# Kernel optimization log

Measured on AMD Instinct MI355X. Metric: run time of the kernel, lower is better.

Reference implementation:

```python
import jax, jax.numpy as jnp
import numpy as np

TEMPERATURE = 0.07


def setup_inputs() -> dict:
    key = jax.random.key(0)
    embeddings = jax.random.normal(key, (16384, 256), dtype=jnp.float32)
    return {"embeddings": embeddings}


def reference(embeddings) -> jnp.ndarray:
    # L2 normalize rows (torch F.normalize uses eps clamp 1e-12)
    norm = jnp.maximum(jnp.linalg.norm(embeddings, axis=1, keepdims=True), 1e-12)
    emb = embeddings / norm
    # [N, N] similarity, temperature-scaled logits
    logits = jnp.matmul(emb, emb.T) / TEMPERATURE
    # cross entropy against diagonal labels (labels[i] = i)
    logp = jax.nn.log_softmax(logits, axis=1)
    loss = -jnp.mean(jnp.diagonal(logp))
    return loss
```

## Files before the change

kernel.cpp:

```cpp
#include <hip/hip_runtime.h>
#include <hip/hip_bf16.h>

typedef __bf16 bf16;
typedef __attribute__((ext_vector_type(8))) __bf16 bf16x8;
typedef __attribute__((ext_vector_type(4))) __bf16 bf16x4;
typedef __attribute__((ext_vector_type(16))) float f32x16;

#define N_ROWS 16384
#define DIM 256
#define NJC 512
#define LSTRIP 16
#define NSTRIPS 2112
#define SQK1 4.53981608f
#define LN2F 0.69314718056f

#define WS_T_OFF (N_ROWS * DIM * 2)
#define WS_D_OFF (WS_T_OFF + N_ROWS * 4)

#define GLOAD_LDS(g, l)                                        \
    __builtin_amdgcn_global_load_lds(                          \
        (const __attribute__((address_space(1))) void*)(g),    \
        (__attribute__((address_space(3))) void*)(l), 16, 0, 0)

__global__ void __launch_bounds__(256) normalize_kernel(const float* __restrict__ in,
                                                        bf16* __restrict__ out,
                                                        float* __restrict__ Tg,
                                                        float* __restrict__ Dg,
                                                        float* __restrict__ loss_out) {
    if (blockIdx.x == 0 && threadIdx.x == 0) loss_out[0] = 0.0f;
    if (blockIdx.x < 64) Tg[blockIdx.x * 256 + threadIdx.x] = 0.0f;

    const int row  = blockIdx.x * 4 + (threadIdx.x >> 6);
    const int lane = threadIdx.x & 63;
    const float4* rp = (const float4*)(in + (size_t)row * DIM);
    float4 v = rp[lane];
    float ss = v.x * v.x + v.y * v.y + v.z * v.z + v.w * v.w;
#pragma unroll
    for (int m = 1; m < 64; m <<= 1) ss += __shfl_xor(ss, m, 64);
    float inv = SQK1 / fmaxf(sqrtf(ss), 1e-12f);
    bf16x4 o;
    o[0] = (bf16)(v.x * inv);
    o[1] = (bf16)(v.y * inv);
    o[2] = (bf16)(v.z * inv);
    o[3] = (bf16)(v.w * inv);
    *(bf16x4*)(out + (size_t)row * DIM + lane * 4) = o;

    float f0 = (float)o[0], f1 = (float)o[1], f2 = (float)o[2], f3 = (float)o[3];
    float s2 = f0 * f0 + f1 * f1 + f2 * f2 + f3 * f3;
#pragma unroll
    for (int m = 1; m < 64; m <<= 1) s2 += __shfl_xor(s2, m, 64);
    if (lane == 0) Dg[row] = s2;
}

#define TREE16(R, out)                                                     \
    do {                                                                   \
        float w8[8], w4[4], w2[2], w1, g_;                                 \
        _Pragma("unroll") for (int i_ = 0; i_ < 8; ++i_) {                 \
            g_ = (lo & 16) ? R[i_] : R[i_ + 8];                            \
            w8[i_] = ((lo & 16) ? R[i_ + 8] : R[i_]) + __shfl_xor(g_, 16); \
        }                                                                  \
        _Pragma("unroll") for (int i_ = 0; i_ < 4; ++i_) {                 \
            g_ = (lo & 8) ? w8[i_] : w8[i_ + 4];                           \
            w4[i_] = ((lo & 8) ? w8[i_ + 4] : w8[i_]) + __shfl_xor(g_, 8); \
        }                                                                  \
        _Pragma("unroll") for (int i_ = 0; i_ < 2; ++i_) {                 \
            g_ = (lo & 4) ? w4[i_] : w4[i_ + 2];                           \
            w2[i_] = ((lo & 4) ? w4[i_ + 2] : w4[i_]) + __shfl_xor(g_, 4); \
        }                                                                  \
        g_ = (lo & 2) ? w2[0] : w2[1];                                     \
        w1 = ((lo & 2) ? w2[1] : w2[0]) + __shfl_xor(g_, 2);               \
        out = w1 + __shfl_xor(w1, 1);                                      \
    } while (0)

__global__ void __launch_bounds__(256, 4)
loss_kernel(const bf16* __restrict__ A, float* __restrict__ Tg) {
    __shared__ bf16 Bs0[32 * DIM];
    __shared__ bf16 Bs1[32 * DIM];

    const int tid = threadIdx.x;
    const int w  = tid >> 6;
    const int l  = tid & 63;
    const int lo = l & 31, hi = l >> 5;

    int it = 0, rem = blockIdx.x;
    for (;;) {
        const int nch = 32 - (it >> 2);
        if (rem < nch) break;
        rem -= nch;
        ++it;
    }
    const int jc0 = 4 * it + rem * LSTRIP;
    const int jc1 = (jc0 + LSTRIP < NJC) ? (jc0 + LSTRIP) : NJC;

    bf16x8 af[16];
    {
        const bf16* ap = A + (size_t)(it * 128 + w * 32 + lo) * DIM + hi * 8;
#pragma unroll
        for (int k = 0; k < 16; ++k)
            af[k] = *(const volatile bf16x8*)(ap + k * 16);
    }

    float s0[16];
#pragma unroll
    for (int r = 0; r < 16; ++r) s0[r] = 0.f;

    const int s_dma = l & 31;
    const int rl    = l >> 5;
    int vo[4];
#pragma unroll
    for (int q = 0; q < 4; ++q) {
        const int c = (s_dma & 24) | ((s_dma & 7) ^ ((q * 2 + rl) & 7));
        vo[q] = rl * DIM + c * 8;
    }

    const int rbase = lo * DIM;
    const int mx7 = lo & 7;

#define ISSUE(jcn, BUF)                                                      \
    do {                                                                     \
        const bf16* tb_ = A + (size_t)((jcn) * 32 + w * 8) * DIM;            \
        bf16* lb_ = &BUF[(w * 8) * DIM];                                     \
        _Pragma("unroll") for (int q_ = 0; q_ < 4; ++q_) {                   \
            GLOAD_LDS(tb_ + (q_ * 2) * DIM + vo[q_],                         \
                      lb_ + (q_ * 2) * DIM);                                 \
        }                                                                    \
    } while (0)

#define TILE_BODY(BR, BW, jc)                                                \
    do {                                                                     \
        asm volatile("s_barrier" ::: "memory");                              \
        if ((jc) + 1 < jc1) {                                                \
            ISSUE((jc) + 1, BW);                                             \
            asm volatile("s_waitcnt vmcnt(4)" ::: "memory");                 \
        } else {                                                             \
            asm volatile("s_waitcnt vmcnt(0)" ::: "memory");                 \
        }                                                                    \
        asm volatile("s_barrier" ::: "memory");                              \
        f32x16 c0;                                                           \
        _Pragma("unroll") for (int r_ = 0; r_ < 16; ++r_) c0[r_] = 0.f;      \
        __builtin_amdgcn_s_setprio(1);                                       \
        _Pragma("unroll") for (int k_ = 0; k_ < 16; ++k_) {                  \
            const int cc_ = k_ * 2 + hi;                                     \
            const int slot_ = (cc_ & 24) | ((cc_ & 7) ^ mx7);                \
            bf16x8 b_ = *(const bf16x8*)&BR[rbase + slot_ * 8];              \
            c0 = __builtin_amdgcn_mfma_f32_32x32x16_bf16(af[k_], b_, c0, 0, 0, 0); \
        }                                                                    \
        __builtin_amdgcn_s_setprio(0);                                       \
        float cs_ = 0.f;                                                     \
        _Pragma("unroll") for (int r_ = 0; r_ < 16; ++r_) {                  \
            float e_ = __builtin_amdgcn_exp2f(c0[r_]);                       \
            s0[r_] += e_;                                                    \
            cs_ += e_;                                                       \
        }                                                                    \
        cs_ += __shfl_xor(cs_, 32);                                          \
                             \
        if (((jc) >> 2) != it && hi == 0)                                    \
            atomicAdd(&Tg[(jc) * 32 + lo], cs_);                             \
    } while (0)

    ISSUE(jc0, Bs0);
    int jc = jc0;
    while (jc < jc1) {
        TILE_BODY(Bs0, Bs1, jc);
        ++jc;
        if (jc >= jc1) break;
        TILE_BODY(Bs1, Bs0, jc);
        ++jc;
    }

    float t0;
    TREE16(s0, t0);
    const int r = (lo >> 1) & 15;
    const int rowoff = (r & 3) + 8 * (r >> 2) + 4 * hi;
    if ((l & 1) == 0)
        atomicAdd(&Tg[it * 128 + w * 32 + rowoff], t0);
#undef ISSUE
#undef TILE_BODY
}

__global__ void __launch_bounds__(256) final_kernel(const float* __restrict__ Tg,
                                                    const float* __restrict__ Dg,
                                                    float* __restrict__ out) {
    __shared__ float red[4];
    const int i = blockIdx.x * 256 + threadIdx.x;
    float c = LN2F * (__log2f(Tg[i]) - Dg[i]) * (1.0f / (float)N_ROWS);
#pragma unroll
    for (int m = 1; m < 64; m <<= 1) c += __shfl_xor(c, m, 64);
    if ((threadIdx.x & 63) == 0) red[threadIdx.x >> 6] = c;
    __syncthreads();
    if (threadIdx.x == 0)
        atomicAdd(out, red[0] + red[1] + red[2] + red[3]);
}

extern "C" void kernel_launch(void* const* d_in, const int* in_sizes, int n_in,
                              void* d_out, int out_size, void* d_ws, size_t ws_size,
                              hipStream_t stream) {
    const float* emb = (const float*)d_in[0];
    float* out = (float*)d_out;
    bf16* Abf = (bf16*)d_ws;
    float* Tg = (float*)((char*)d_ws + WS_T_OFF);
    float* Dg = (float*)((char*)d_ws + WS_D_OFF);

    hipLaunchKernelGGL(normalize_kernel, dim3(N_ROWS / 4), dim3(256), 0, stream,
                       emb, Abf, Tg, Dg, out);
    hipLaunchKernelGGL(loss_kernel, dim3(NSTRIPS), dim3(256), 0, stream,
                       Abf, Tg);
    hipLaunchKernelGGL(final_kernel, dim3(N_ROWS / 256), dim3(256), 0, stream,
                       Tg, Dg, out);
}
```

Measured before the change: 161.6 us.

## Use stream-K style even tile partitioning across fixed block count

New measurement: 156.3 us. 1.03x faster.

```diff
diff --git a/kernel.cpp b/kernel.cpp
--- a/kernel.cpp
+++ b/kernel.cpp
@@ -9,8 +9,8 @@
 #define N_ROWS 16384
 #define DIM 256
 #define NJC 512
-#define LSTRIP 16
-#define NSTRIPS 2112
+#define NBLKS 1024
+#define NTILES 33024
 #define SQK1 4.53981608f
 #define LN2F 0.69314718056f
 
@@ -82,23 +82,22 @@
     const int l  = tid & 63;
     const int lo = l & 31, hi = l >> 5;
 
-    int it = 0, rem = blockIdx.x;
-    for (;;) {
-        const int nch = 32 - (it >> 2);
-        if (rem < nch) break;
-        rem -= nch;
-        ++it;
-    }
-    const int jc0 = 4 * it + rem * LSTRIP;
-    const int jc1 = (jc0 + LSTRIP < NJC) ? (jc0 + LSTRIP) : NJC;
+    const int tbeg = (int)(((unsigned)blockIdx.x * 129u) >> 2);
+    const int tend = (int)((((unsigned)blockIdx.x + 1u) * 129u) >> 2);
+    const int nrem = tend - tbeg;
+
+    int it = 0;
+    while (2 * (it + 1) * (257 - (it + 1)) <= tbeg) ++it;
+    int jc = 4 * it + (tbeg - 2 * it * (257 - it));
 
     bf16x8 af[16];
-    {
-        const bf16* ap = A + (size_t)(it * 128 + w * 32 + lo) * DIM + hi * 8;
-#pragma unroll
-        for (int k = 0; k < 16; ++k)
-            af[k] = *(const volatile bf16x8*)(ap + k * 16);
-    }
+#define LOAD_AF                                                              \
+    do {                                                                     \
+        const bf16* ap_ = A + (size_t)(it * 128 + w * 32 + lo) * DIM + hi * 8; \
+        _Pragma("unroll") for (int k_ = 0; k_ < 16; ++k_)                    \
+            af[k_] = *(const volatile bf16x8*)(ap_ + k_ * 16);               \
+    } while (0)
+    LOAD_AF;
 
     float s0[16];
 #pragma unroll
@@ -116,9 +115,9 @@
     const int rbase = lo * DIM;
     const int mx7 = lo & 7;
 
-#define ISSUE(jcn, BUF)                                                      \
-    do {                                                                     \
-        const bf16* tb_ = A + (size_t)((jcn) * 32 + w * 8) * DIM;            \
+#define ISSUE(jcn_, BUF)                                                     \
+    do {                                                                     \
+        const bf16* tb_ = A + (size_t)((jcn_) * 32 + w * 8) * DIM;           \
         bf16* lb_ = &BUF[(w * 8) * DIM];                                     \
         _Pragma("unroll") for (int q_ = 0; q_ < 4; ++q_) {                   \
             GLOAD_LDS(tb_ + (q_ * 2) * DIM + vo[q_],                         \
@@ -126,14 +125,36 @@
         }                                                                    \
     } while (0)
 
-#define TILE_BODY(BR, BW, jc)                                                \
+#define FLUSH_ROWS                                                           \
+    do {                                                                     \
+        float tr_;                                                           \
+        TREE16(s0, tr_);                                                     \
+        const int r_ = (lo >> 1) & 15;                                       \
+        const int rowoff_ = (r_ & 3) + 8 * (r_ >> 2) + 4 * hi;               \
+        if ((l & 1) == 0)                                                    \
+            atomicAdd(&Tg[it * 128 + w * 32 + rowoff_], tr_);                \
+    } while (0)
+
+    int t = 0, jcn, itn;
+    bool has_next;
+
+#define NEXT_DECODE                                                          \
+    do {                                                                     \
+        has_next = (t + 1 < nrem);                                           \
+        if (has_next) {                                                      \
+            jcn = jc + 1; itn = it;                                          \
+            if (jcn == NJC) { itn = it + 1; jcn = 4 * itn; }                 \
+        } else { jcn = jc; itn = it; }                                       \
+    } while (0)
+
+#define TILE_BODY(BR, BW, WN, WL)                                            \
     do {                                                                     \
         asm volatile("s_barrier" ::: "memory");                              \
-        if ((jc) + 1 < jc1) {                                                \
-            ISSUE((jc) + 1, BW);                                             \
-            asm volatile("s_waitcnt vmcnt(4)" ::: "memory");                 \
+        if (has_next) {                                                      \
+            ISSUE(jcn, BW);                                                  \
+            asm volatile("s_waitcnt vmcnt(" #WN ")" ::: "memory");           \
         } else {                                                             \
-            asm volatile("s_waitcnt vmcnt(0)" ::: "memory");                 \
+            asm volatile("s_waitcnt vmcnt(" #WL ")" ::: "memory");           \
         }                                                                    \
         asm volatile("s_barrier" ::: "memory");                              \
         f32x16 c0;                                                           \
@@ -153,29 +174,45 @@
             cs_ += e_;                                                       \
         }                                                                    \
         cs_ += __shfl_xor(cs_, 32);                                          \
-                             \
-        if (((jc) >> 2) != it && hi == 0)                                    \
-            atomicAdd(&Tg[(jc) * 32 + lo], cs_);                             \
-    } while (0)
-
-    ISSUE(jc0, Bs0);
-    int jc = jc0;
-    while (jc < jc1) {
-        TILE_BODY(Bs0, Bs1, jc);
-        ++jc;
-        if (jc >= jc1) break;
-        TILE_BODY(Bs1, Bs0, jc);
-        ++jc;
+         \
+         \
+        const float fv_ = ((jc >> 2) == it) ? 0.0f : cs_;                    \
+        if (hi == 0) atomicAdd(&Tg[jc * 32 + lo], fv_);                      \
+    } while (0)
+
+#define ADVANCE                                                              \
+    do {                                                                     \
+        ++t;                                                                 \
+        if (itn != it) {                                                     \
+            FLUSH_ROWS;                                                      \
+            it = itn;                                                        \
+            LOAD_AF;                                                         \
+            _Pragma("unroll") for (int r_ = 0; r_ < 16; ++r_) s0[r_] = 0.f;  \
+        }                                                                    \
+        jc = jcn;                                                            \
+    } while (0)
+
+    ISSUE(jc, Bs0);
+    NEXT_DECODE;
+    TILE_BODY(Bs0, Bs1, 4, 0);
+    ADVANCE;
+    while (t < nrem) {
+        NEXT_DECODE;
+        TILE_BODY(Bs1, Bs0, 5, 1);
+        ADVANCE;
+        if (t >= nrem) break;
+        NEXT_DECODE;
+        TILE_BODY(Bs0, Bs1, 5, 1);
+        ADVANCE;
     }
-
-    float t0;
-    TREE16(s0, t0);
-    const int r = (lo >> 1) & 15;
-    const int rowoff = (r & 3) + 8 * (r >> 2) + 4 * hi;
-    if ((l & 1) == 0)
-        atomicAdd(&Tg[it * 128 + w * 32 + rowoff], t0);
+    FLUSH_ROWS;
+
 #undef ISSUE
 #undef TILE_BODY
+#undef NEXT_DECODE
+#undef ADVANCE
+#undef FLUSH_ROWS
+#undef LOAD_AF
 }
 
 __global__ void __launch_bounds__(256) final_kernel(const float* __restrict__ Tg,
@@ -203,7 +240,7 @@
 
     hipLaunchKernelGGL(normalize_kernel, dim3(N_ROWS / 4), dim3(256), 0, stream,
                        emb, Abf, Tg, Dg, out);
-    hipLaunchKernelGGL(loss_kernel, dim3(NSTRIPS), dim3(256), 0, stream,
+    hipLaunchKernelGGL(loss_kernel, dim3(NBLKS), dim3(256), 0, stream,
                        Abf, Tg);
     hipLaunchKernelGGL(final_kernel, dim3(N_ROWS / 256), dim3(256), 0, stream,
                        Tg, Dg, out);
```
